# Kernel optimization log

Measured on AMD Instinct MI355X. Metric: run time of the kernel, lower is better.

Reference implementation:

```python
import jax, jax.numpy as jnp
import numpy as np

NEG_SLOPE = 0.2  # PyG GATConv default negative_slope


def gat_conv(x, W, a_src, a_dst, bias, src, dst, heads, out_c, concat):
    """PyG-style GATConv with self-loops. x:[N,F_in], W:[F_in,heads*out_c]."""
    N = x.shape[0]
    # add self loops
    loop = jnp.arange(N, dtype=src.dtype)
    src = jnp.concatenate([src, loop])
    dst = jnp.concatenate([dst, loop])
    h = (x @ W).reshape(N, heads, out_c)            # [N,H,C]
    alpha_src = jnp.sum(h * a_src, axis=-1)          # [N,H]
    alpha_dst = jnp.sum(h * a_dst, axis=-1)          # [N,H]
    e = jax.nn.leaky_relu(alpha_src[src] + alpha_dst[dst], NEG_SLOPE)  # [E,H]
    # segment softmax over incoming edges of each destination node
    m = jax.ops.segment_max(e, dst, num_segments=N)  # [N,H]
    ex = jnp.exp(e - m[dst])
    s = jax.ops.segment_sum(ex, dst, num_segments=N)
    alpha = ex / (s[dst] + 1e-16)                    # [E,H]
    msg = h[src] * alpha[:, :, None]                 # [E,H,C]
    out = jax.ops.segment_sum(msg, dst, num_segments=N)  # [N,H,C]
    out = out.reshape(N, heads * out_c) if concat else out.mean(axis=1)
    return out + bias


def setup_inputs() -> dict:
    key = jax.random.key(0)
    ks = jax.random.split(key, 16)
    N, E = 25000, 400000
    node_dim, hidden, out_dim, heads = 64, 128, 256, 4

    def glorot(k, shape):
        fan = shape[0] + shape[-1]
        return jax.random.normal(k, shape, jnp.float32) * np.sqrt(2.0 / fan)

    return {
        "x": jax.random.normal(ks[0], (N, node_dim), jnp.float32),
        "edge_index": jax.random.randint(ks[1], (2, E), 0, N, jnp.int32),
        "W_emb": glorot(ks[2], (node_dim, hidden)),
        "b_emb": jnp.zeros((hidden,), jnp.float32),
        "W1": glorot(ks[3], (hidden, heads * hidden)),
        "a1_src": glorot(ks[4], (heads, hidden)),
        "a1_dst": glorot(ks[5], (heads, hidden)),
        "b1": jnp.zeros((heads * hidden,), jnp.float32),
        "W2": glorot(ks[6], (heads * hidden, hidden)),
        "a2_src": glorot(ks[7], (1, hidden)),
        "a2_dst": glorot(ks[8], (1, hidden)),
        "b2": jnp.zeros((hidden,), jnp.float32),
        "W_out": glorot(ks[9], (hidden, out_dim)),
        "b_out": jnp.zeros((out_dim,), jnp.float32),
    }


def reference(x, edge_index, W_emb, b_emb, W1, a1_src, a1_dst, b1, W2, a2_src, a2_dst, b2, W_out, b_out):
    src, dst = edge_index[0], edge_index[1]
    heads, hidden = a1_src.shape[0], a1_src.shape[1]
    h = jax.nn.relu(x @ W_emb + b_emb)                 # dropout is identity in eval
    h = gat_conv(h, W1, a1_src, a1_dst, b1, src, dst, heads, hidden, True)
    h = jax.nn.elu(h)
    h = gat_conv(h, W2, a2_src, a2_dst, b2, src, dst, 1, hidden, False)
    h = jax.nn.elu(h)
    g = jnp.mean(h, axis=0, keepdims=True)             # global mean pool, batch=None -> [1, hidden]
    return g @ W_out + b_out                           # [1, out_dim]
```

## Files before the change

kernel.cpp:

```cpp
#include <hip/hip_runtime.h>
#include <hip/hip_bf16.h>


#define LRELU(x) ((x) > 0.f ? (x) : 0.2f * (x))

typedef short bf16x8 __attribute__((ext_vector_type(8)));
typedef float f32x4 __attribute__((ext_vector_type(4)));
typedef float f32x2 __attribute__((ext_vector_type(2)));

static __device__ __forceinline__ unsigned short f2b(float f) {
    union { float f; unsigned u; } x; x.f = f;
    unsigned r = x.u + 0x7fff + ((x.u >> 16) & 1);
    return (unsigned short)(r >> 16);
}
static __device__ __forceinline__ float rl_f(float v, int c) {
    return __int_as_float(__builtin_amdgcn_readlane(__float_as_int(v), c));
}
static __device__ __forceinline__ unsigned char f2fp8(float v) {
    int p = __builtin_amdgcn_cvt_pk_fp8_f32(v, v, 0, false);
    return (unsigned char)(p & 0xff);
}

__global__ void zero_kernel(int* __restrict__ deg, int* __restrict__ cursor,
                            float* __restrict__ pool, int* __restrict__ done, int N) {
    int i = blockIdx.x * blockDim.x + threadIdx.x;
    if (i < N) deg[i] = 0;
    else if (i < 2 * N) cursor[i - N] = 0;
    else if (i < 2 * N + 128) pool[i - 2 * N] = 0.f;
    else if (i == 2 * N + 128) *done = 0;
}

__global__ void deg_count_kernel(const int* __restrict__ ei, int E, int N, int* __restrict__ deg) {
    int i = blockIdx.x * blockDim.x + threadIdx.x;
    if (i < E) atomicAdd(&deg[ei[E + i]], 1);
    else if (i < E + N) atomicAdd(&deg[i - E], 1);
}

__global__ __launch_bounds__(256) void scan_pass1(const int* __restrict__ deg, int* __restrict__ rowptr,
                                                  int* __restrict__ bsum, int N) {
    __shared__ int sd[256];
    int t = threadIdx.x, i = blockIdx.x * 256 + t;
    int d = (i < N) ? deg[i] : 0;
    sd[t] = d;
    __syncthreads();
    for (int off = 1; off < 256; off <<= 1) {
        int v = (t >= off) ? sd[t - off] : 0;
        __syncthreads();
        sd[t] += v;
        __syncthreads();
    }
    if (i < N) rowptr[i] = sd[t] - d;
    if (t == 255) bsum[blockIdx.x] = sd[t];
}

__global__ __launch_bounds__(128) void scan_pass2(const int* __restrict__ bsum, int* __restrict__ boff,
                                                  int* __restrict__ rowptr, int nb, int N) {
    __shared__ int sd[128];
    int t = threadIdx.x;
    int d = (t < nb) ? bsum[t] : 0;
    sd[t] = d;
    __syncthreads();
    for (int off = 1; off < 128; off <<= 1) {
        int v = (t >= off) ? sd[t - off] : 0;
        __syncthreads();
        sd[t] += v;
        __syncthreads();
    }
    if (t < nb) boff[t] = sd[t] - d;
    if (t == 127) rowptr[N] = sd[t];
}

__global__ __launch_bounds__(256) void scan_pass3(int* __restrict__ rowptr, const int* __restrict__ boff, int N) {
    int i = blockIdx.x * 256 + threadIdx.x;
    if (i < N) rowptr[i] += boff[blockIdx.x];
}

__global__ void scatter_kernel(const int* __restrict__ ei, int E, int N,
                               const int* __restrict__ rowptr, int* __restrict__ cursor,
                               int* __restrict__ esrc) {
    int i = blockIdx.x * blockDim.x + threadIdx.x;
    int s, d;
    if (i < E) { s = ei[i]; d = ei[E + i]; }
    else if (i < E + N) { s = i - E; d = s; }
    else return;
    int pos = rowptr[d] + atomicAdd(&cursor[d], 1);
    esrc[pos] = s;
}

__global__ void prep_kernel(const float* __restrict__ x, const float* __restrict__ We,
                            const float* __restrict__ W1, const float* __restrict__ W2,
                            unsigned short* __restrict__ xb, unsigned short* __restrict__ WeT,
                            unsigned short* __restrict__ W1T, unsigned short* __restrict__ W2T,
                            int Nx) {
    int i = blockIdx.x * blockDim.x + threadIdx.x;
    if (i < Nx) { xb[i] = f2b(x[i]); return; }
    i -= Nx;
    if (i < 64 * 128) { int k = i >> 7, n = i & 127; WeT[n * 64 + k] = f2b(We[i]); return; }
    i -= 64 * 128;
    if (i < 128 * 512) { int k = i >> 9, n = i & 511; W1T[n * 128 + k] = f2b(W1[i]); return; }
    i -= 128 * 512;
    if (i < 512 * 128) { int k = i >> 7, n = i & 127; W2T[n * 512 + k] = f2b(W2[i]); return; }
}

template <int ACT, int OFMT, int ALPHA, int H>
__global__ __launch_bounds__(256) void gemm_mfma_nt(const unsigned short* __restrict__ A,
                                                    const unsigned short* __restrict__ Bt,
                                                    const float* __restrict__ bias,
                                                    void* __restrict__ Cout,
                                                    const float* __restrict__ a_src,
                                                    const float* __restrict__ a_dst,
                                                    float* __restrict__ as_out,
                                                    float* __restrict__ ad_out,
                                                    int M, int N, int K) {
    __shared__ __align__(16) unsigned short As[128 * 40];
    __shared__ __align__(16) unsigned short Bs[128 * 40];
    __shared__ float sAl[128][2];
    int tid = threadIdx.x;
    int gm0 = blockIdx.y * 128, gn0 = blockIdx.x * 128;
    int w = tid >> 6, lane = tid & 63;
    int wrow = (w >> 1) * 64, wcol = (w & 1) * 64;
    int l15 = lane & 15, quad = lane >> 4;

    f32x4 acc[4][4];
#pragma unroll
    for (int i = 0; i < 4; i++)
#pragma unroll
        for (int j = 0; j < 4; j++) acc[i][j] = {0.f, 0.f, 0.f, 0.f};

    for (int k0 = 0; k0 < K; k0 += 32) {
#pragma unroll
        for (int rr = 0; rr < 2; rr++) {
            int lin = tid + rr * 256;
            int row = lin >> 2;
            int cg = (lin & 3) * 8;
            int grow = gm0 + row; if (grow >= M) grow = M - 1;
            uint4 va = *(const uint4*)&A[(size_t)grow * K + k0 + cg];
            *(uint4*)&As[row * 40 + cg] = va;
            uint4 vb = *(const uint4*)&Bt[(size_t)(gn0 + row) * K + k0 + cg];
            *(uint4*)&Bs[row * 40 + cg] = vb;
        }
        __syncthreads();
        bf16x8 af[4], bfr[4];
#pragma unroll
        for (int i = 0; i < 4; i++) {
            af[i]  = *(const bf16x8*)&As[(wrow + i * 16 + l15) * 40 + quad * 8];
            bfr[i] = *(const bf16x8*)&Bs[(wcol + i * 16 + l15) * 40 + quad * 8];
        }
#pragma unroll
        for (int i = 0; i < 4; i++)
#pragma unroll
            for (int j = 0; j < 4; j++)
                acc[i][j] = __builtin_amdgcn_mfma_f32_16x16x32_bf16(af[i], bfr[j], acc[i][j], 0, 0, 0);
        __syncthreads();
    }

    if (OFMT == 0) {
        unsigned short* C = (unsigned short*)Cout;
#pragma unroll
        for (int i = 0; i < 4; i++) {
            int row = gm0 + wrow + i * 16 + quad * 4;
#pragma unroll
            for (int j = 0; j < 4; j++) {
                int col = gn0 + wcol + j * 16 + l15;
                float bv = bias ? bias[col] : 0.f;
#pragma unroll
                for (int r = 0; r < 4; r++) {
                    int gr = row + r;
                    if (gr < M) {
                        float v = acc[i][j][r] + bv;
                        if (ACT == 1) v = fmaxf(v, 0.f);
                        C[(size_t)gr * N + col] = f2b(v);
                    }
                }
            }
        }
    } else {
        unsigned char* C8 = (unsigned char*)Cout;
#pragma unroll
        for (int i = 0; i < 4; i++) {
            int row = gm0 + wrow + i * 16 + quad * 4;
#pragma unroll
            for (int j = 0; j < 4; j++) {
                int col = gn0 + wcol + j * 16 + l15;
#pragma unroll
                for (int r = 0; r < 4; r++) {
                    int gr = row + r;
                    if (gr < M) C8[(size_t)gr * N + col] = f2fp8(acc[i][j][r]);
                }
            }
        }
    }

    if (ALPHA) {
        int hh = blockIdx.x;
        float as_c[4], ad_c[4];
#pragma unroll
        for (int j = 0; j < 4; j++) {
            int c = gn0 + wcol + j * 16 + l15;
            as_c[j] = a_src[c];
            ad_c[j] = a_dst[c];
        }
#pragma unroll
        for (int i = 0; i < 4; i++) {
#pragma unroll
            for (int r = 0; r < 4; r++) {
                float ps = 0.f, pd = 0.f;
#pragma unroll
                for (int j = 0; j < 4; j++) {
                    ps += acc[i][j][r] * as_c[j];
                    pd += acc[i][j][r] * ad_c[j];
                }
#pragma unroll
                for (int o = 1; o < 16; o <<= 1) {
                    ps += __shfl_xor(ps, o);
                    pd += __shfl_xor(pd, o);
                }
                if (wcol == 64 && l15 == 0) {
                    int lr = wrow + i * 16 + quad * 4 + r;
                    sAl[lr][0] = ps;
                    sAl[lr][1] = pd;
                }
            }
        }
        __syncthreads();
        if (wcol == 0) {
#pragma unroll
            for (int i = 0; i < 4; i++) {
#pragma unroll
                for (int r = 0; r < 4; r++) {
                    float ps = 0.f, pd = 0.f;
#pragma unroll
                    for (int j = 0; j < 4; j++) {
                        ps += acc[i][j][r] * as_c[j];
                        pd += acc[i][j][r] * ad_c[j];
                    }
#pragma unroll
                    for (int o = 1; o < 16; o <<= 1) {
                        ps += __shfl_xor(ps, o);
                        pd += __shfl_xor(pd, o);
                    }
                    if (l15 == 0) {
                        int lr = wrow + i * 16 + quad * 4 + r;
                        int gr = gm0 + lr;
                        if (gr < M) {
                            as_out[(size_t)gr * H + hh] = ps + sAl[lr][0];
                            ad_out[(size_t)gr * H + hh] = pd + sAl[lr][1];
                        }
                    }
                }
            }
        }
    }
}

__global__ __launch_bounds__(256) void gat_agg_l1(const unsigned* __restrict__ hq,
                                                  const float4* __restrict__ as4,
                                                  const float4* __restrict__ ad4,
                                                  const int* __restrict__ rowptr,
                                                  const int* __restrict__ esrc,
                                                  const float* __restrict__ bias,
                                                  unsigned short* __restrict__ out, int N) {
    __shared__ float wlds_all[4][256];
    int w = threadIdx.x >> 6, lane = threadIdx.x & 63;
    int n = blockIdx.x * 4 + w;
    if (n >= N) return;
    float* wlds = wlds_all[w];
    int begin = rowptr[n], deg = rowptr[n + 1] - begin;
    float4 adn = ad4[n];

    int s_l0 = 0;
    float4 e0 = {-3.4e38f, -3.4e38f, -3.4e38f, -3.4e38f};
    if (lane < deg) {
        s_l0 = esrc[begin + lane];
        float4 u = as4[s_l0];
        e0.x = LRELU(u.x + adn.x); e0.y = LRELU(u.y + adn.y);
        e0.z = LRELU(u.z + adn.z); e0.w = LRELU(u.w + adn.w);
    }
    float4 m = e0;
    for (int base = 64; base < deg; base += 64) {
        int j = base + lane;
        if (j < deg) {
            float4 u = as4[esrc[begin + j]];
            m.x = fmaxf(m.x, LRELU(u.x + adn.x)); m.y = fmaxf(m.y, LRELU(u.y + adn.y));
            m.z = fmaxf(m.z, LRELU(u.z + adn.z)); m.w = fmaxf(m.w, LRELU(u.w + adn.w));
        }
    }
#pragma unroll
    for (int o = 32; o >= 1; o >>= 1) {
        m.x = fmaxf(m.x, __shfl_xor(m.x, o));
        m.y = fmaxf(m.y, __shfl_xor(m.y, o));
        m.z = fmaxf(m.z, __shfl_xor(m.z, o));
        m.w = fmaxf(m.w, __shfl_xor(m.w, o));
    }
    float4 s4 = {0.f, 0.f, 0.f, 0.f};
    if (lane < deg) {
        s4.x = __expf(e0.x - m.x); s4.y = __expf(e0.y - m.y);
        s4.z = __expf(e0.z - m.z); s4.w = __expf(e0.w - m.w);
    }
    for (int base = 64; base < deg; base += 64) {
        int j = base + lane;
        if (j < deg) {
            float4 u = as4[esrc[begin + j]];
            s4.x += __expf(LRELU(u.x + adn.x) - m.x); s4.y += __expf(LRELU(u.y + adn.y) - m.y);
            s4.z += __expf(LRELU(u.z + adn.z) - m.z); s4.w += __expf(LRELU(u.w + adn.w) - m.w);
        }
    }
#pragma unroll
    for (int o = 32; o >= 1; o >>= 1) {
        s4.x += __shfl_xor(s4.x, o); s4.y += __shfl_xor(s4.y, o);
        s4.z += __shfl_xor(s4.z, o); s4.w += __shfl_xor(s4.w, o);
    }
    float4 inv = {1.f / (s4.x + 1e-16f), 1.f / (s4.y + 1e-16f),
                  1.f / (s4.z + 1e-16f), 1.f / (s4.w + 1e-16f)};

    float acc[8] = {};
    int h = lane >> 4;
#define ACC_E1(q, wgt) { \
    f32x2 p0 = __builtin_amdgcn_cvt_pk_f32_fp8((int)q.x, false); \
    f32x2 p1 = __builtin_amdgcn_cvt_pk_f32_fp8((int)q.x, true);  \
    f32x2 p2 = __builtin_amdgcn_cvt_pk_f32_fp8((int)q.y, false); \
    f32x2 p3 = __builtin_amdgcn_cvt_pk_f32_fp8((int)q.y, true);  \
    acc[0] += wgt * p0.x; acc[1] += wgt * p0.y; acc[2] += wgt * p1.x; acc[3] += wgt * p1.y; \
    acc[4] += wgt * p2.x; acc[5] += wgt * p2.y; acc[6] += wgt * p3.x; acc[7] += wgt * p3.y; }

    for (int base = 0; base < deg; base += 64) {
        int j = base + lane;
        int len = min(64, deg - base);
        int s_l = s_l0;
        float4 e = e0;
        if (base > 0 && j < deg) {
            s_l = esrc[begin + j];
            float4 u = as4[s_l];
            e.x = LRELU(u.x + adn.x); e.y = LRELU(u.y + adn.y);
            e.z = LRELU(u.z + adn.z); e.w = LRELU(u.w + adn.w);
        }
        if (j < deg) {
            float4 wv4 = {__expf(e.x - m.x) * inv.x, __expf(e.y - m.y) * inv.y,
                          __expf(e.z - m.z) * inv.z, __expf(e.w - m.w) * inv.w};
            *(float4*)&wlds[lane * 4] = wv4;
        }
        int c = 0;
        for (; c + 4 <= len; c += 4) {
            int s0 = __builtin_amdgcn_readlane(s_l, c);
            int s1 = __builtin_amdgcn_readlane(s_l, c + 1);
            int s2 = __builtin_amdgcn_readlane(s_l, c + 2);
            int s3 = __builtin_amdgcn_readlane(s_l, c + 3);
            uint2 q0 = *((const uint2*)(hq + (size_t)s0 * 128) + lane);
            uint2 q1 = *((const uint2*)(hq + (size_t)s1 * 128) + lane);
            uint2 q2 = *((const uint2*)(hq + (size_t)s2 * 128) + lane);
            uint2 q3 = *((const uint2*)(hq + (size_t)s3 * 128) + lane);
            float w0 = wlds[c * 4 + h];
            float w1 = wlds[c * 4 + 4 + h];
            float w2 = wlds[c * 4 + 8 + h];
            float w3 = wlds[c * 4 + 12 + h];
            ACC_E1(q0, w0); ACC_E1(q1, w1); ACC_E1(q2, w2); ACC_E1(q3, w3);
        }
        for (; c < len; c++) {
            int s0 = __builtin_amdgcn_readlane(s_l, c);
            uint2 q0 = *((const uint2*)(hq + (size_t)s0 * 128) + lane);
            float w0 = wlds[c * 4 + h];
            ACC_E1(q0, w0);
        }
    }
#undef ACC_E1
    int f0 = lane * 8;
    unsigned pk[4];
#pragma unroll
    for (int k = 0; k < 4; k++) {
        float v0 = acc[2 * k] + bias[f0 + 2 * k];
        float v1 = acc[2 * k + 1] + bias[f0 + 2 * k + 1];
        v0 = v0 > 0.f ? v0 : (__expf(v0) - 1.f);
        v1 = v1 > 0.f ? v1 : (__expf(v1) - 1.f);
        pk[k] = (unsigned)f2b(v0) | ((unsigned)f2b(v1) << 16);
    }
    uint4 pv = {pk[0], pk[1], pk[2], pk[3]};
    *((uint4*)(out + (size_t)n * 512) + lane) = pv;
}

__global__ __launch_bounds__(256) void gat_agg_l2(const unsigned char* __restrict__ hq,
                                                  const float* __restrict__ as,
                                                  const float* __restrict__ ad,
                                                  const int* __restrict__ rowptr,
                                                  const int* __restrict__ esrc,
                                                  const float* __restrict__ bias,
                                                  float* __restrict__ out, int N) {
    int w = threadIdx.x >> 6, lane = threadIdx.x & 63;
    int n = blockIdx.x * 4 + w;
    if (n >= N) return;
    int begin = rowptr[n], deg = rowptr[n + 1] - begin;
    float adn = ad[n];

    int s_l0 = 0;
    float e0 = -3.4e38f;
    if (lane < deg) {
        s_l0 = esrc[begin + lane];
        e0 = LRELU(as[s_l0] + adn);
    }
    float m = e0;
    for (int base = 64; base < deg; base += 64) {
        int j = base + lane;
        if (j < deg) m = fmaxf(m, LRELU(as[esrc[begin + j]] + adn));
    }
#pragma unroll
    for (int o = 32; o >= 1; o >>= 1) m = fmaxf(m, __shfl_xor(m, o));

    float s = (lane < deg) ? __expf(e0 - m) : 0.f;
    for (int base = 64; base < deg; base += 64) {
        int j = base + lane;
        if (j < deg) s += __expf(LRELU(as[esrc[begin + j]] + adn) - m);
    }
#pragma unroll
    for (int o = 32; o >= 1; o >>= 1) s += __shfl_xor(s, o);
    float inv = 1.f / (s + 1e-16f);

    float acc0 = 0.f, acc1 = 0.f;
    for (int base = 0; base < deg; base += 64) {
        int j = base + lane;
        int len = min(64, deg - base);
        int s_l = s_l0;
        float e = e0;
        if (base > 0 && j < deg) {
            s_l = esrc[begin + j];
            e = LRELU(as[s_l] + adn);
        }
        float w_l = (j < deg) ? __expf(e - m) * inv : 0.f;
        int c = 0;
        for (; c + 4 <= len; c += 4) {
            int sp0 = __builtin_amdgcn_readlane(s_l, c);
            int sp1 = __builtin_amdgcn_readlane(s_l, c + 1);
            int sp2 = __builtin_amdgcn_readlane(s_l, c + 2);
            int sp3 = __builtin_amdgcn_readlane(s_l, c + 3);
            unsigned short u0 = *((const unsigned short*)(hq + (size_t)sp0 * 128) + lane);
            unsigned short u1 = *((const unsigned short*)(hq + (size_t)sp1 * 128) + lane);
            unsigned short u2 = *((const unsigned short*)(hq + (size_t)sp2 * 128) + lane);
            unsigned short u3 = *((const unsigned short*)(hq + (size_t)sp3 * 128) + lane);
            float w0 = rl_f(w_l, c), w1 = rl_f(w_l, c + 1);
            float w2 = rl_f(w_l, c + 2), w3 = rl_f(w_l, c + 3);
            f32x2 p0 = __builtin_amdgcn_cvt_pk_f32_fp8((int)u0, false);
            f32x2 p1 = __builtin_amdgcn_cvt_pk_f32_fp8((int)u1, false);
            f32x2 p2 = __builtin_amdgcn_cvt_pk_f32_fp8((int)u2, false);
            f32x2 p3 = __builtin_amdgcn_cvt_pk_f32_fp8((int)u3, false);
            acc0 += w0 * p0.x; acc1 += w0 * p0.y;
            acc0 += w1 * p1.x; acc1 += w1 * p1.y;
            acc0 += w2 * p2.x; acc1 += w2 * p2.y;
            acc0 += w3 * p3.x; acc1 += w3 * p3.y;
        }
        for (; c < len; c++) {
            int sp0 = __builtin_amdgcn_readlane(s_l, c);
            float w0 = rl_f(w_l, c);
            unsigned short u0 = *((const unsigned short*)(hq + (size_t)sp0 * 128) + lane);
            f32x2 p0 = __builtin_amdgcn_cvt_pk_f32_fp8((int)u0, false);
            acc0 += w0 * p0.x; acc1 += w0 * p0.y;
        }
    }
    float v0 = acc0 + bias[lane * 2];
    float v1 = acc1 + bias[lane * 2 + 1];
    v0 = v0 > 0.f ? v0 : (__expf(v0) - 1.f);
    v1 = v1 > 0.f ? v1 : (__expf(v1) - 1.f);
    float2 pv = {v0, v1};
    *(float2*)&out[(size_t)n * 128 + lane * 2] = pv;
}

__global__ __launch_bounds__(256) void pool_final_kernel(const float* __restrict__ o2,
                                                         float* __restrict__ pool,
                                                         int* __restrict__ done,
                                                         const float* __restrict__ Wout,
                                                         const float* __restrict__ bout,
                                                         float* __restrict__ out,
                                                         int N, int nblocks, float invN) {
    __shared__ float4 sred[256];
    int f4 = threadIdx.x & 31;
    int r = blockIdx.x * 256 + (threadIdx.x >> 5);
    float4 acc = {0.f, 0.f, 0.f, 0.f};
    for (int i = 0; i < 32; i++, r += 8) {
        if (r < N) {
            float4 v = *(const float4*)&o2[(size_t)r * 128 + f4 * 4];
            acc.x += v.x; acc.y += v.y; acc.z += v.z; acc.w += v.w;
        }
    }
    sred[threadIdx.x] = acc;
    __syncthreads();
    if (threadIdx.x < 32) {
        float4 t = sred[threadIdx.x];
#pragma unroll
        for (int k = 1; k < 8; k++) {
            float4 u = sred[threadIdx.x + 32 * k];
            t.x += u.x; t.y += u.y; t.z += u.z; t.w += u.w;
        }
        atomicAdd(&pool[f4 * 4 + 0], t.x);
        atomicAdd(&pool[f4 * 4 + 1], t.y);
        atomicAdd(&pool[f4 * 4 + 2], t.z);
        atomicAdd(&pool[f4 * 4 + 3], t.w);
    }
    __threadfence();
    __shared__ int isLast;
    if (threadIdx.x == 0) isLast = (atomicAdd(done, 1) == nblocks - 1);
    __syncthreads();
    if (isLast) {
        __shared__ float spool[128];
        if (threadIdx.x < 128) spool[threadIdx.x] = atomicAdd(&pool[threadIdx.x], 0.f);
        __syncthreads();
        int o = threadIdx.x;
        float a = 0.f;
        for (int k = 0; k < 128; k++) a += spool[k] * Wout[k * 256 + o];
        out[o] = a * invN + bout[o];
    }
}

extern "C" void kernel_launch(void* const* d_in, const int* in_sizes, int n_in,
                              void* d_out, int out_size, void* d_ws, size_t ws_size,
                              hipStream_t stream) {
    const float* x      = (const float*)d_in[0];
    const int*   ei     = (const int*)d_in[1];
    const float* W_emb  = (const float*)d_in[2];
    const float* b_emb  = (const float*)d_in[3];
    const float* W1     = (const float*)d_in[4];
    const float* a1_src = (const float*)d_in[5];
    const float* a1_dst = (const float*)d_in[6];
    const float* b1     = (const float*)d_in[7];
    const float* W2     = (const float*)d_in[8];
    const float* a2_src = (const float*)d_in[9];
    const float* a2_dst = (const float*)d_in[10];
    const float* b2     = (const float*)d_in[11];
    const float* W_out  = (const float*)d_in[12];
    const float* b_out  = (const float*)d_in[13];
    float* out = (float*)d_out;

    const int N = in_sizes[0] / 64;
    const int E = in_sizes[1] / 2;
    const int Etot = E + N;
    const int nb = (N + 255) / 256;

    char* ws = (char*)d_ws;
    size_t off = 0;
    auto alloc = [&](size_t bytes) -> void* {
        void* p = ws + off;
        off = (off + bytes + 255) & ~(size_t)255;
        return p;
    };
    typedef unsigned short u16;
    u16* xb    = (u16*)alloc((size_t)N * 64 * 2);
    u16* WeT   = (u16*)alloc((size_t)128 * 64 * 2);
    u16* W1T   = (u16*)alloc((size_t)512 * 128 * 2);
    u16* W2T   = (u16*)alloc((size_t)128 * 512 * 2);
    u16* h0b   = (u16*)alloc((size_t)N * 128 * 2);
    unsigned char* h1q = (unsigned char*)alloc((size_t)N * 512);
    u16* o1b   = (u16*)alloc((size_t)N * 512 * 2);
    unsigned char* h2q = (unsigned char*)alloc((size_t)N * 128);
    float* o2  = (float*)alloc((size_t)N * 128 * 4);
    float* as1 = (float*)alloc((size_t)N * 4 * 4);
    float* ad1 = (float*)alloc((size_t)N * 4 * 4);
    float* as2 = (float*)alloc((size_t)N * 4);
    float* ad2 = (float*)alloc((size_t)N * 4);
    float* pool = (float*)alloc(128 * 4);
    int* done   = (int*)alloc(256);
    int* rowptr = (int*)alloc((size_t)(N + 1) * 4);
    int* deg    = (int*)alloc((size_t)N * 4);
    int* cursor = (int*)alloc((size_t)N * 4);
    int* bsum   = (int*)alloc(128 * 4);
    int* boff   = (int*)alloc(128 * 4);
    int* esrc   = (int*)alloc((size_t)Etot * 4);

    zero_kernel<<<(2 * N + 129 + 255) / 256, 256, 0, stream>>>(deg, cursor, pool, done, N);
    int blocksE = (Etot + 255) / 256;
    deg_count_kernel<<<blocksE, 256, 0, stream>>>(ei, E, N, deg);
    scan_pass1<<<nb, 256, 0, stream>>>(deg, rowptr, bsum, N);
    scan_pass2<<<1, 128, 0, stream>>>(bsum, boff, rowptr, nb, N);
    scan_pass3<<<nb, 256, 0, stream>>>(rowptr, boff, N);
    scatter_kernel<<<blocksE, 256, 0, stream>>>(ei, E, N, rowptr, cursor, esrc);

    int Nx = N * 64;
    int prep_elems = Nx + 64 * 128 + 128 * 512 + 512 * 128;
    prep_kernel<<<(prep_elems + 255) / 256, 256, 0, stream>>>(x, W_emb, W1, W2, xb, WeT, W1T, W2T, Nx);

    int mtiles = (N + 127) / 128;
    gemm_mfma_nt<1, 0, 0, 1><<<dim3(1, mtiles), 256, 0, stream>>>(
        xb, WeT, b_emb, h0b, nullptr, nullptr, nullptr, nullptr, N, 128, 64);
    gemm_mfma_nt<0, 1, 1, 4><<<dim3(4, mtiles), 256, 0, stream>>>(
        h0b, W1T, nullptr, h1q, a1_src, a1_dst, as1, ad1, N, 512, 128);

    gat_agg_l1<<<(N + 3) / 4, 256, 0, stream>>>((const unsigned*)h1q, (const float4*)as1,
                                                (const float4*)ad1, rowptr, esrc, b1, o1b, N);

    gemm_mfma_nt<0, 1, 1, 1><<<dim3(1, mtiles), 256, 0, stream>>>(
        o1b, W2T, nullptr, h2q, a2_src, a2_dst, as2, ad2, N, 128, 512);

    gat_agg_l2<<<(N + 3) / 4, 256, 0, stream>>>(h2q, as2, ad2, rowptr, esrc, b2, o2, N);

    int npb = (N + 255) / 256;
    pool_final_kernel<<<npb, 256, 0, stream>>>(o2, pool, done, W_out, b_out, out,
                                               N, npb, 1.f / (float)N);
}
```

Baseline: 280.5 us.

## Fuse embedding GEMM into layer-1 GEMM keeping hidden tile in shared memory

```diff
diff --git a/kernel.cpp b/kernel.cpp
--- a/kernel.cpp
+++ b/kernel.cpp
@@ -100,6 +100,179 @@
     if (i < 128 * 512) { int k = i >> 9, n = i & 511; W1T[n * 128 + k] = f2b(W1[i]); return; }
     i -= 128 * 512;
     if (i < 512 * 128) { int k = i >> 7, n = i & 127; W2T[n * 512 + k] = f2b(W2[i]); return; }
+}
+
+__global__ __launch_bounds__(256) void gemm12_fused(const unsigned short* __restrict__ A,
+                                                    const unsigned short* __restrict__ WeT,
+                                                    const float* __restrict__ b_emb,
+                                                    const unsigned short* __restrict__ W1T,
+                                                    unsigned char* __restrict__ C8,
+                                                    const float* __restrict__ a_src,
+                                                    const float* __restrict__ a_dst,
+                                                    float* __restrict__ as_out,
+                                                    float* __restrict__ ad_out, int M) {
+    __shared__ __align__(16) unsigned short smem[22016];
+    unsigned short* Asx = smem;
+    unsigned short* Bwe = smem + 9216;
+    unsigned short* h0s = smem;
+    unsigned short* Bs  = smem + 16896;
+    __shared__ float sAl[128][2];
+
+    int tid = threadIdx.x;
+    int gm0 = blockIdx.y * 128, gn0 = blockIdx.x * 128;
+    int w = tid >> 6, lane = tid & 63;
+    int wrow = (w >> 1) * 64, wcol = (w & 1) * 64;
+    int l15 = lane & 15, quad = lane >> 4;
+
+    f32x4 acc[4][4];
+#pragma unroll
+    for (int i = 0; i < 4; i++)
+#pragma unroll
+        for (int j = 0; j < 4; j++) acc[i][j] = {0.f, 0.f, 0.f, 0.f};
+
+#pragma unroll
+    for (int rr = 0; rr < 4; rr++) {
+        int lin = tid + rr * 256;
+        int row = lin >> 3;
+        int cg = (lin & 7) * 8;
+        int grow = gm0 + row; if (grow >= M) grow = M - 1;
+        *(uint4*)&Asx[row * 72 + cg] = *(const uint4*)&A[(size_t)grow * 64 + cg];
+        *(uint4*)&Bwe[row * 72 + cg] = *(const uint4*)&WeT[(size_t)row * 64 + cg];
+    }
+    __syncthreads();
+#pragma unroll
+    for (int k0 = 0; k0 < 64; k0 += 32) {
+        bf16x8 af[4], bfr[4];
+#pragma unroll
+        for (int i = 0; i < 4; i++) {
+            af[i]  = *(const bf16x8*)&Asx[(wrow + i * 16 + l15) * 72 + k0 + quad * 8];
+            bfr[i] = *(const bf16x8*)&Bwe[(wcol + i * 16 + l15) * 72 + k0 + quad * 8];
+        }
+#pragma unroll
+        for (int i = 0; i < 4; i++)
+#pragma unroll
+            for (int j = 0; j < 4; j++)
+                acc[i][j] = __builtin_amdgcn_mfma_f32_16x16x32_bf16(af[i], bfr[j], acc[i][j], 0, 0, 0);
+    }
+    __syncthreads();
+
+#pragma unroll
+    for (int j = 0; j < 4; j++) {
+        int col = wcol + j * 16 + l15;
+        float bv = b_emb[col];
+#pragma unroll
+        for (int i = 0; i < 4; i++) {
+            int row = wrow + i * 16 + quad * 4;
+#pragma unroll
+            for (int r = 0; r < 4; r++) {
+                float v = fmaxf(acc[i][j][r] + bv, 0.f);
+                h0s[(row + r) * 132 + col] = f2b(v);
+            }
+        }
+    }
+
+#pragma unroll
+    for (int i = 0; i < 4; i++)
+#pragma unroll
+        for (int j = 0; j < 4; j++) acc[i][j] = {0.f, 0.f, 0.f, 0.f};
+
+    for (int k0 = 0; k0 < 128; k0 += 32) {
+#pragma unroll
+        for (int rr = 0; rr < 2; rr++) {
+            int lin = tid + rr * 256;
+            int row = lin >> 2;
+            int cg = (lin & 3) * 8;
+            *(uint4*)&Bs[row * 40 + cg] = *(const uint4*)&W1T[(size_t)(gn0 + row) * 128 + k0 + cg];
+        }
+        __syncthreads();
+        bf16x8 af[4], bfr[4];
+#pragma unroll
+        for (int i = 0; i < 4; i++) {
+            af[i]  = *(const bf16x8*)&h0s[(wrow + i * 16 + l15) * 132 + k0 + quad * 8];
+            bfr[i] = *(const bf16x8*)&Bs[(wcol + i * 16 + l15) * 40 + quad * 8];
+        }
+#pragma unroll
+        for (int i = 0; i < 4; i++)
+#pragma unroll
+            for (int j = 0; j < 4; j++)
+                acc[i][j] = __builtin_amdgcn_mfma_f32_16x16x32_bf16(af[i], bfr[j], acc[i][j], 0, 0, 0);
+        __syncthreads();
+    }
+
+#pragma unroll
+    for (int i = 0; i < 4; i++) {
+        int row = gm0 + wrow + i * 16 + quad * 4;
+#pragma unroll
+        for (int j = 0; j < 4; j++) {
+            int col = gn0 + wcol + j * 16 + l15;
+#pragma unroll
+            for (int r = 0; r < 4; r++) {
+                int gr = row + r;
+                if (gr < M) C8[(size_t)gr * 512 + col] = f2fp8(acc[i][j][r]);
+            }
+        }
+    }
+
+    {
+        int hh = blockIdx.x;
+        float as_c[4], ad_c[4];
+#pragma unroll
+        for (int j = 0; j < 4; j++) {
+            int c = gn0 + wcol + j * 16 + l15;
+            as_c[j] = a_src[c];
+            ad_c[j] = a_dst[c];
+        }
+#pragma unroll
+        for (int i = 0; i < 4; i++) {
+#pragma unroll
+            for (int r = 0; r < 4; r++) {
+                float ps = 0.f, pd = 0.f;
+#pragma unroll
+                for (int j = 0; j < 4; j++) {
+                    ps += acc[i][j][r] * as_c[j];
+                    pd += acc[i][j][r] * ad_c[j];
+                }
+#pragma unroll
+                for (int o = 1; o < 16; o <<= 1) {
+                    ps += __shfl_xor(ps, o);
+                    pd += __shfl_xor(pd, o);
+                }
+                if (wcol == 64 && l15 == 0) {
+                    int lr = wrow + i * 16 + quad * 4 + r;
+                    sAl[lr][0] = ps;
+                    sAl[lr][1] = pd;
+                }
+            }
+        }
+        __syncthreads();
+        if (wcol == 0) {
+#pragma unroll
+            for (int i = 0; i < 4; i++) {
+#pragma unroll
+                for (int r = 0; r < 4; r++) {
+                    float ps = 0.f, pd = 0.f;
+#pragma unroll
+                    for (int j = 0; j < 4; j++) {
+                        ps += acc[i][j][r] * as_c[j];
+                        pd += acc[i][j][r] * ad_c[j];
+                    }
+#pragma unroll
+                    for (int o = 1; o < 16; o <<= 1) {
+                        ps += __shfl_xor(ps, o);
+                        pd += __shfl_xor(pd, o);
+                    }
+                    if (l15 == 0) {
+                        int lr = wrow + i * 16 + quad * 4 + r;
+                        int gr = gm0 + lr;
+                        if (gr < M) {
+                            as_out[(size_t)gr * 4 + hh] = ps + sAl[lr][0];
+                            ad_out[(size_t)gr * 4 + hh] = pd + sAl[lr][1];
+                        }
+                    }
+                }
+            }
+        }
+    }
 }
 
 template <int ACT, int OFMT, int ALPHA, int H>
@@ -543,7 +716,6 @@
     u16* WeT   = (u16*)alloc((size_t)128 * 64 * 2);
     u16* W1T   = (u16*)alloc((size_t)512 * 128 * 2);
     u16* W2T   = (u16*)alloc((size_t)128 * 512 * 2);
-    u16* h0b   = (u16*)alloc((size_t)N * 128 * 2);
     unsigned char* h1q = (unsigned char*)alloc((size_t)N * 512);
     u16* o1b   = (u16*)alloc((size_t)N * 512 * 2);
     unsigned char* h2q = (unsigned char*)alloc((size_t)N * 128);
@@ -574,10 +746,8 @@
     prep_kernel<<<(prep_elems + 255) / 256, 256, 0, stream>>>(x, W_emb, W1, W2, xb, WeT, W1T, W2T, Nx);
 
     int mtiles = (N + 127) / 128;
-    gemm_mfma_nt<1, 0, 0, 1><<<dim3(1, mtiles), 256, 0, stream>>>(
-        xb, WeT, b_emb, h0b, nullptr, nullptr, nullptr, nullptr, N, 128, 64);
-    gemm_mfma_nt<0, 1, 1, 4><<<dim3(4, mtiles), 256, 0, stream>>>(
-        h0b, W1T, nullptr, h1q, a1_src, a1_dst, as1, ad1, N, 512, 128);
+    gemm12_fused<<<dim3(4, mtiles), 256, 0, stream>>>(xb, WeT, b_emb, W1T, h1q,
+                                                      a1_src, a1_dst, as1, ad1, N);
 
     gat_agg_l1<<<(N + 3) / 4, 256, 0, stream>>>((const unsigned*)h1q, (const float4*)as1,
                                                 (const float4*)ad1, rowptr, esrc, b1, o1b, N);
```

Result: no change. 277.3 us (-1.2%).
